# Kernel tuning notes

Measured on AMD Instinct MI355X. Metric: run time of the kernel, lower is better.

## Reference

```python
import jax, jax.numpy as jnp
import numpy as np

N_EMBD = 1024
HEAD_SIZE = 64

def setup_inputs() -> dict:
    key = jax.random.key(0)
    k1, k2, k3, k4 = jax.random.split(key, 4)
    x = jax.random.normal(k1, (8, 2048, N_EMBD), dtype=jnp.float32)
    s = 1.0 / np.sqrt(N_EMBD)
    Wk = jax.random.normal(k2, (HEAD_SIZE, N_EMBD), dtype=jnp.float32) * s
    Wq = jax.random.normal(k3, (HEAD_SIZE, N_EMBD), dtype=jnp.float32) * s
    Wv = jax.random.normal(k4, (HEAD_SIZE, N_EMBD), dtype=jnp.float32) * s
    return {"x": x, "Wk": Wk, "Wq": Wq, "Wv": Wv}

def reference(x, Wk, Wq, Wv):
    B, T, C = x.shape
    k = jnp.einsum('btc,hc->bth', x, Wk)  # [B,T,Hd]
    q = jnp.einsum('btc,hc->bth', x, Wq)
    v = jnp.einsum('btc,hc->bth', x, Wv)
    # NOTE: original scales by C**-0.5 where C = n_embd (not head_size)
    wei = jnp.einsum('bqh,bkh->bqk', q, k) * (C ** -0.5)  # [B,T,T]
    causal = jnp.tril(jnp.ones((T, T), dtype=bool))
    wei = jnp.where(causal, wei, -jnp.inf)
    wei = jax.nn.softmax(wei, axis=-1)
    out = jnp.einsum('bqk,bkh->bqh', wei, v)  # [B,T,Hd]
    return out
```

## Files before the change

kernel.cpp:

```cpp
#include <hip/hip_runtime.h>


typedef __attribute__((ext_vector_type(4))) short sv4;
typedef __attribute__((ext_vector_type(8))) short sv8;
typedef __attribute__((ext_vector_type(4))) float f32x4;

#define NB   8
#define TSEQ 2048
#define CDIM 1024
#define HD   64
#define MROWS (NB * TSEQ)

__device__ __forceinline__ short f2s(float f) {
  union { float f; unsigned u; } v; v.f = f;
  unsigned u = v.u;
  u += 0x7fffu + ((u >> 16) & 1u);
  return (short)(u >> 16);
}
__device__ __forceinline__ unsigned pk2(float lo, float hi) {
  return (unsigned)(unsigned short)f2s(lo) | ((unsigned)(unsigned short)f2s(hi) << 16);
}
__device__ __forceinline__ void glds16(const short* g, short* l) {
  __builtin_amdgcn_global_load_lds(
      (const __attribute__((address_space(1))) unsigned int*)g,
      (__attribute__((address_space(3))) unsigned int*)l, 16, 0, 0);
}

__global__ __launch_bounds__(256) void wcvt(
    const float* __restrict__ Wq, const float* __restrict__ Wk,
    const float* __restrict__ Wv, short* __restrict__ wb)
{
  int i = blockIdx.x * 256 + threadIdx.x;
  int t = i / 3072;
  int rem = i - t * 3072;
  int r = rem >> 4, s = rem & 15;
  int j = r >> 6, wrow = r & 63;
  const float* W = (j == 0) ? Wq : (j == 1) ? Wk : Wv;
  const float* src = W + (size_t)wrow * CDIM + t * 128 + ((s ^ (wrow & 7)) << 3);
  float4 a = *(const float4*)src;
  float4 b = *(const float4*)(src + 4);
  sv8 v = {f2s(a.x), f2s(a.y), f2s(a.z), f2s(a.w),
           f2s(b.x), f2s(b.y), f2s(b.z), f2s(b.w)};
  *(sv8*)(wb + (size_t)i * 8) = v;
}

__global__ __launch_bounds__(1024) void qkv_proj(
    const float* __restrict__ x,
    const short* __restrict__ wb,
    short* __restrict__ qw,
    short* __restrict__ kw,
    short* __restrict__ vtw)
{
  __shared__ short wlds[2][24576];
  __shared__ short xlds[2][8192];
  const int tid  = threadIdx.x;
  const int wid  = tid >> 6;
  const int lane = tid & 63;
  const int g    = lane >> 4;
  const int c16  = lane & 15;
  const int rowg = wid >> 2;
  const int ph   = wid & 3;
  const int row0 = blockIdx.x * 64;

  const int xr = tid >> 4, xs = tid & 15;
  const float* xsrc = x + (size_t)(row0 + xr) * CDIM + xs * 8;
  const int xwo = xr * 128 + ((xs ^ (xr & 7)) << 3);

  const int arow = rowg * 16 + c16;
  const int x7   = arow & 7;
  int rWo[3], rW7[3];
  #pragma unroll
  for (int p6 = 0; p6 < 3; ++p6) {
    int p = ph * 3 + p6;
    int r = (p >> 2) * 64 + (p & 3) * 16 + c16;
    rWo[p6] = r * 128;
    rW7[p6] = r & 7;
  }

  f32x4 acc[3];
  #pragma unroll
  for (int p6 = 0; p6 < 3; ++p6) acc[p6] = (f32x4){0.f, 0.f, 0.f, 0.f};

  float4 px[2][2];

  #pragma unroll
  for (int k2 = 0; k2 < 3; ++k2)
    glds16(wb + (size_t)(tid + k2 * 1024) * 8, &wlds[0][(tid + k2 * 1024) * 8]);
  px[0][0] = *(const float4*)(xsrc);
  px[0][1] = *(const float4*)(xsrc + 4);
  px[1][0] = *(const float4*)(xsrc + 128);
  px[1][1] = *(const float4*)(xsrc + 132);
  asm volatile("s_waitcnt vmcnt(2)" ::: "memory");
  {
    float4 A = px[0][0], B = px[0][1];
    sv8 v = {f2s(A.x), f2s(A.y), f2s(A.z), f2s(A.w),
             f2s(B.x), f2s(B.y), f2s(B.z), f2s(B.w)};
    *(sv8*)&xlds[0][xwo] = v;
  }
  asm volatile("s_waitcnt lgkmcnt(0)" ::: "memory");
  __builtin_amdgcn_sched_barrier(0);
  __builtin_amdgcn_s_barrier();

  #pragma unroll
  for (int t = 0; t < 8; ++t) {
    const int buf = t & 1;
    if (t < 7) {
      #pragma unroll
      for (int k2 = 0; k2 < 3; ++k2)
        glds16(wb + (size_t)((t + 1) * 3072 + tid + k2 * 1024) * 8,
               &wlds[buf ^ 1][(tid + k2 * 1024) * 8]);
    }
    if (t < 6) {
      px[t & 1][0] = *(const float4*)(xsrc + (t + 2) * 128);
      px[t & 1][1] = *(const float4*)(xsrc + (t + 2) * 128 + 4);
    }
    if (t < 7) {
      float4 A = px[(t + 1) & 1][0], B = px[(t + 1) & 1][1];
      sv8 v = {f2s(A.x), f2s(A.y), f2s(A.z), f2s(A.w),
               f2s(B.x), f2s(B.y), f2s(B.z), f2s(B.w)};
      *(sv8*)&xlds[buf ^ 1][xwo] = v;
    }
    #pragma unroll
    for (int kk = 0; kk < 4; ++kk) {
      int kslot = kk * 4 + g;
      sv8 a = *(const sv8*)&xlds[buf][arow * 128 + ((kslot ^ x7) << 3)];
      #pragma unroll
      for (int p6 = 0; p6 < 3; ++p6) {
        sv8 bfr = *(const sv8*)&wlds[buf][rWo[p6] + ((kslot ^ rW7[p6]) << 3)];
        acc[p6] = __builtin_amdgcn_mfma_f32_16x16x32_bf16(a, bfr, acc[p6], 0, 0, 0);
      }
    }
    if (t < 7) {
      if (t < 6) asm volatile("s_waitcnt vmcnt(2) lgkmcnt(0)" ::: "memory");
      else       asm volatile("s_waitcnt vmcnt(0) lgkmcnt(0)" ::: "memory");
      __builtin_amdgcn_sched_barrier(0);
      __builtin_amdgcn_s_barrier();
    }
  }

  #pragma unroll
  for (int p6 = 0; p6 < 3; ++p6) {
    int p = ph * 3 + p6, j = p >> 2, n = p & 3;
    int cc  = (n << 4) + c16;
    int rr0 = row0 + rowg * 16 + (g << 2);
    if (j == 2) {
      int b = rr0 >> 11, ti = rr0 & (TSEQ - 1);
      int kt = ti >> 6, key = ti & 63;
      sv4 v = {f2s(acc[p6][0]), f2s(acc[p6][1]), f2s(acc[p6][2]), f2s(acc[p6][3])};
      *(sv4*)&vtw[(((size_t)b * 32 + kt) * 64 + cc) * 64 +
                  ((((key >> 3) ^ (cc & 7)) << 3) | (key & 7))] = v;
    } else {
      #pragma unroll
      for (int r = 0; r < 4; ++r) {
        int rr = rr0 + r;
        if (j == 0) {
          qw[(size_t)rr * HD + cc] = f2s(acc[p6][r] * 0.03125f);
        } else {
          kw[(size_t)rr * HD + ((((cc >> 3) ^ (rr & 7)) << 3) | (cc & 7))] =
              f2s(acc[p6][r]);
        }
      }
    }
  }
}

__global__ __launch_bounds__(512, 4) void attn(
    const short* __restrict__ qw,
    const short* __restrict__ kw,
    const short* __restrict__ vtw,
    float* __restrict__ Opart,
    float* __restrict__ mlws)
{
  __shared__ short kbuf[2][8192];
  __shared__ short vbuf[2][8192];
  __shared__ short bridge[8][1024];

  const int tid  = threadIdx.x;
  const int wid  = tid >> 6;
  const int lane = tid & 63;
  const int g    = lane >> 4;
  const int c16  = lane & 15;

  const int bid   = blockIdx.x;
  const int batch = bid & 7;
  const int jb    = (bid >> 3) & 15;
  const int qt    = bid >> 7;
  const int q0    = jb << 7;
  const size_t base = (size_t)batch * TSEQ * HD;

  const int ntot = jb + 1;
  const int t0   = (ntot * qt) >> 2;
  const int t1   = (ntot * (qt + 1)) >> 2;

  const int qrow = q0 + (wid << 4) + c16;
  sv8 qa0 = *(const sv8*)(qw + base + (size_t)qrow * HD + (g << 3));
  sv8 qa1 = *(const sv8*)(qw + base + (size_t)qrow * HD + 32 + (g << 3));

  float m = -1e30f, l = 0.f;
  f32x4 o[4];
  #pragma unroll
  for (int n = 0; n < 4; ++n) o[n] = (f32x4){0.f, 0.f, 0.f, 0.f};

  short* br = &bridge[wid][0];
  const int sx7 = c16 & 7;

  #define STAGE(tt, bb)                                                      \
    {                                                                        \
      const short* ksrc = kw + base + (size_t)(tt) * 8192;                   \
      const short* vsrc = vtw + ((size_t)batch * 32 + (tt) * 2) * 4096;      \
      glds16(ksrc + tid * 8,         &kbuf[bb][tid * 8]);                    \
      glds16(ksrc + (512 + tid) * 8, &kbuf[bb][(512 + tid) * 8]);            \
      glds16(vsrc + tid * 8,         &vbuf[bb][tid * 8]);                    \
      glds16(vsrc + (512 + tid) * 8, &vbuf[bb][(512 + tid) * 8]);            \
    }

  if (t0 < t1) {
    STAGE(t0, 0);
    asm volatile("s_waitcnt vmcnt(0)" ::: "memory");
    __builtin_amdgcn_s_barrier();

    for (int t = t0; t < t1; ++t) {
      const int buf = (t - t0) & 1;
      if (t + 1 < t1) STAGE(t + 1, buf ^ 1);

      f32x4 s[8];
      #pragma unroll
      for (int n = 0; n < 8; ++n) s[n] = (f32x4){0.f, 0.f, 0.f, 0.f};
      __builtin_amdgcn_s_setprio(1);
      #pragma unroll
      for (int n = 0; n < 8; ++n) {
        int kr = (n << 4) + c16;
        sv8 k0 = *(const sv8*)&kbuf[buf][kr * 64 + ((g ^ (kr & 7)) << 3)];
        s[n] = __builtin_amdgcn_mfma_f32_16x16x32_bf16(k0, qa0, s[n], 0, 0, 0);
        sv8 k1 = *(const sv8*)&kbuf[buf][kr * 64 + (((4 + g) ^ (kr & 7)) << 3)];
        s[n] = __builtin_amdgcn_mfma_f32_16x16x32_bf16(k1, qa1, s[n], 0, 0, 0);
      }
      __builtin_amdgcn_s_setprio(0);

      if (t == jb) {
        #pragma unroll
        for (int n = 0; n < 8; ++n) {
          int key = (t << 7) + (n << 4) + (g << 2);
          #pragma unroll
          for (int r = 0; r < 4; ++r)
            s[n][r] = (key + r <= qrow) ? s[n][r] : -1e30f;
        }
      }

      float mx = -1e30f;
      #pragma unroll
      for (int n = 0; n < 8; ++n)
        mx = fmaxf(mx, fmaxf(fmaxf(s[n][0], s[n][1]), fmaxf(s[n][2], s[n][3])));
      mx = fmaxf(mx, __shfl_xor(mx, 16));
      mx = fmaxf(mx, __shfl_xor(mx, 32));
      float mnew  = fmaxf(m, mx);
      float alpha = __expf(m - mnew);
      m = mnew;

      float sum = 0.f;
      #pragma unroll
      for (int n = 0; n < 8; ++n) {
        float p0 = __expf(s[n][0] - mnew);
        float p1 = __expf(s[n][1] - mnew);
        float p2 = __expf(s[n][2] - mnew);
        float p3 = __expf(s[n][3] - mnew);
        s[n][0] = p0; s[n][1] = p1; s[n][2] = p2; s[n][3] = p3;
        sum += (p0 + p1) + (p2 + p3);
      }
      sum += __shfl_xor(sum, 16);
      sum += __shfl_xor(sum, 32);
      l = l * alpha + sum;

      float af[4];
      #pragma unroll
      for (int r = 0; r < 4; ++r) af[r] = __shfl(alpha, (g << 2) + r);
      #pragma unroll
      for (int n = 0; n < 4; ++n)
        #pragma unroll
        for (int r = 0; r < 4; ++r) o[n][r] *= af[r];

      #pragma unroll
      for (int hv = 0; hv < 2; ++hv) {
        #pragma unroll
        for (int n = 0; n < 4; ++n) {
          int nn = (hv << 2) + n;
          int slot = 2 * n + (g >> 1);
          uint2 w2;
          w2.x = pk2(s[nn][0], s[nn][1]);
          w2.y = pk2(s[nn][2], s[nn][3]);
          *(uint2*)&br[(c16 << 6) + ((slot ^ sx7) << 3) + ((g & 1) << 2)] = w2;
        }
        asm volatile("s_waitcnt lgkmcnt(0)" ::: "memory");
        __builtin_amdgcn_sched_barrier(0);
        __builtin_amdgcn_s_setprio(1);
        #pragma unroll
        for (int kk = 0; kk < 2; ++kk) {
          int kg    = (hv << 1) + kk;
          int kslot = (kg << 2) + g;
          sv8 pa = *(const sv8*)&br[(c16 << 6) + ((((kk << 2) + g) ^ sx7) << 3)];
          #pragma unroll
          for (int n = 0; n < 4; ++n) {
            int vr = (n << 4) + c16;
            sv8 vf = *(const sv8*)&vbuf[buf][(kslot >> 3) * 4096 + vr * 64 +
                                             (((kslot & 7) ^ (vr & 7)) << 3)];
            o[n] = __builtin_amdgcn_mfma_f32_16x16x32_bf16(pa, vf, o[n], 0, 0, 0);
          }
        }
        __builtin_amdgcn_s_setprio(0);
      }

      if (t + 1 < t1) {
        asm volatile("s_waitcnt vmcnt(0)" ::: "memory");
        __builtin_amdgcn_sched_barrier(0);
        __builtin_amdgcn_s_barrier();
      }
    }
  }

  #pragma unroll
  for (int n = 0; n < 4; ++n) {
    #pragma unroll
    for (int r = 0; r < 4; ++r) {
      int row = (wid << 4) + (g << 2) + r;
      Opart[(size_t)bid * 8192 + row * 64 + (n << 4) + c16] = o[n][r];
    }
  }
  if (lane < 16) {
    int row = (wid << 4) + lane;
    mlws[((size_t)bid * 128 + row) * 2]     = m;
    mlws[((size_t)bid * 128 + row) * 2 + 1] = l;
  }
  #undef STAGE
}

__global__ __launch_bounds__(256) void combine(
    const float* __restrict__ Opart,
    const float* __restrict__ mlws,
    float* __restrict__ out)
{
  const int bid   = blockIdx.x;
  const int batch = bid & 7;
  const int jb    = (bid >> 3) & 15;
  const int half  = bid >> 7;
  const int tid   = threadIdx.x;
  const int row   = (half << 6) + (tid >> 2);
  const int cs    = (tid & 3) << 4;
  const int pb0   = (jb << 3) + batch;

  float mq[4], lq[4];
  #pragma unroll
  for (int q = 0; q < 4; ++q) {
    int pb = (q << 7) + pb0;
    mq[q] = mlws[((size_t)pb * 128 + row) * 2];
    lq[q] = mlws[((size_t)pb * 128 + row) * 2 + 1];
  }
  float M = fmaxf(fmaxf(mq[0], mq[1]), fmaxf(mq[2], mq[3]));
  float w[4], L = 0.f;
  #pragma unroll
  for (int q = 0; q < 4; ++q) { w[q] = __expf(mq[q] - M); L += w[q] * lq[q]; }
  float invL = 1.f / L;

  float* op = out + ((size_t)batch * TSEQ + (jb << 7) + row) * HD + cs;
  #pragma unroll
  for (int e = 0; e < 4; ++e) {
    float4 acc = {0.f, 0.f, 0.f, 0.f};
    #pragma unroll
    for (int q = 0; q < 4; ++q) {
      int pb = (q << 7) + pb0;
      float4 v = *(const float4*)(Opart + (size_t)pb * 8192 + row * 64 + cs + e * 4);
      acc.x += v.x * w[q]; acc.y += v.y * w[q];
      acc.z += v.z * w[q]; acc.w += v.w * w[q];
    }
    acc.x *= invL; acc.y *= invL; acc.z *= invL; acc.w *= invL;
    *(float4*)(op + e * 4) = acc;
  }
}

extern "C" void kernel_launch(void* const* d_in, const int* in_sizes, int n_in,
                              void* d_out, int out_size, void* d_ws, size_t ws_size,
                              hipStream_t stream) {
  const float* x  = (const float*)d_in[0];
  const float* Wk = (const float*)d_in[1];
  const float* Wq = (const float*)d_in[2];
  const float* Wv = (const float*)d_in[3];
  float* out = (float*)d_out;

  short* qw  = (short*)d_ws;
  short* kw  = qw + (size_t)MROWS * HD;
  short* vtw = kw + (size_t)MROWS * HD;
  short* wb  = vtw + (size_t)NB * HD * TSEQ;
  float* Opart = (float*)(wb + 24576 * 8);
  float* mlws  = Opart + (size_t)512 * 8192;

  wcvt<<<dim3(96), dim3(256), 0, stream>>>(Wq, Wk, Wv, wb);
  qkv_proj<<<dim3(MROWS / 64), dim3(1024), 0, stream>>>(x, wb, qw, kw, vtw);
  attn<<<dim3(512), dim3(512), 0, stream>>>(qw, kw, vtw, Opart, mlws);
  combine<<<dim3(256), dim3(256), 0, stream>>>(Opart, mlws, out);
}
```

Before: 52.29 us.

## Give each attention wave two 16-row query tiles, halving block size

The attention block shrinks from 8 waves to 4. Each wave now owns 32 query rows as two 16-row tiles, so every K and V fragment loaded from LDS feeds two MFMAs instead of one. Each thread issues four async K/V copies instead of two, and the P bridge buffer is reorganised per wave. The aim is to cut LDS read traffic per MFMA and raise instruction-level parallelism. The cost is roughly double the accumulator registers per wave and fewer waves to hide latency, which may reduce occupancy.

```diff
diff --git a/kernel.cpp b/kernel.cpp
--- a/kernel.cpp
+++ b/kernel.cpp
@@ -164,7 +164,7 @@
   }
 }
 
-__global__ __launch_bounds__(512, 4) void attn(
+__global__ __launch_bounds__(256) void attn(
     const short* __restrict__ qw,
     const short* __restrict__ kw,
     const short* __restrict__ vtw,
@@ -173,7 +173,7 @@
 {
   __shared__ short kbuf[2][8192];
   __shared__ short vbuf[2][8192];
-  __shared__ short bridge[8][1024];
+  __shared__ short bridge[4][2048];
 
   const int tid  = threadIdx.x;
   const int wid  = tid >> 6;
@@ -192,14 +192,20 @@
   const int t0   = (ntot * qt) >> 2;
   const int t1   = (ntot * (qt + 1)) >> 2;
 
-  const int qrow = q0 + (wid << 4) + c16;
-  sv8 qa0 = *(const sv8*)(qw + base + (size_t)qrow * HD + (g << 3));
-  sv8 qa1 = *(const sv8*)(qw + base + (size_t)qrow * HD + 32 + (g << 3));
-
-  float m = -1e30f, l = 0.f;
-  f32x4 o[4];
-  #pragma unroll
-  for (int n = 0; n < 4; ++n) o[n] = (f32x4){0.f, 0.f, 0.f, 0.f};
+  const int qrA = q0 + (wid << 5) + c16;
+  const int qrB = qrA + 16;
+  sv8 qa0A = *(const sv8*)(qw + base + (size_t)qrA * HD + (g << 3));
+  sv8 qa1A = *(const sv8*)(qw + base + (size_t)qrA * HD + 32 + (g << 3));
+  sv8 qa0B = *(const sv8*)(qw + base + (size_t)qrB * HD + (g << 3));
+  sv8 qa1B = *(const sv8*)(qw + base + (size_t)qrB * HD + 32 + (g << 3));
+
+  float mA = -1e30f, lA = 0.f, mB = -1e30f, lB = 0.f;
+  f32x4 oA[4], oB[4];
+  #pragma unroll
+  for (int n = 0; n < 4; ++n) {
+    oA[n] = (f32x4){0.f, 0.f, 0.f, 0.f};
+    oB[n] = (f32x4){0.f, 0.f, 0.f, 0.f};
+  }
 
   short* br = &bridge[wid][0];
   const int sx7 = c16 & 7;
@@ -208,10 +214,12 @@
     {                                                                        \
       const short* ksrc = kw + base + (size_t)(tt) * 8192;                   \
       const short* vsrc = vtw + ((size_t)batch * 32 + (tt) * 2) * 4096;      \
-      glds16(ksrc + tid * 8,         &kbuf[bb][tid * 8]);                    \
-      glds16(ksrc + (512 + tid) * 8, &kbuf[bb][(512 + tid) * 8]);            \
-      glds16(vsrc + tid * 8,         &vbuf[bb][tid * 8]);                    \
-      glds16(vsrc + (512 + tid) * 8, &vbuf[bb][(512 + tid) * 8]);            \
+      _Pragma("unroll")                                                      \
+      for (int q = 0; q < 4; ++q)                                            \
+        glds16(ksrc + (tid + q * 256) * 8, &kbuf[bb][(tid + q * 256) * 8]);  \
+      _Pragma("unroll")                                                      \
+      for (int q = 0; q < 4; ++q)                                            \
+        glds16(vsrc + (tid + q * 256) * 8, &vbuf[bb][(tid + q * 256) * 8]);  \
     }
 
   if (t0 < t1) {
@@ -223,17 +231,22 @@
       const int buf = (t - t0) & 1;
       if (t + 1 < t1) STAGE(t + 1, buf ^ 1);
 
-      f32x4 s[8];
-      #pragma unroll
-      for (int n = 0; n < 8; ++n) s[n] = (f32x4){0.f, 0.f, 0.f, 0.f};
+      f32x4 sA[8], sB[8];
+      #pragma unroll
+      for (int n = 0; n < 8; ++n) {
+        sA[n] = (f32x4){0.f, 0.f, 0.f, 0.f};
+        sB[n] = (f32x4){0.f, 0.f, 0.f, 0.f};
+      }
       __builtin_amdgcn_s_setprio(1);
       #pragma unroll
       for (int n = 0; n < 8; ++n) {
         int kr = (n << 4) + c16;
         sv8 k0 = *(const sv8*)&kbuf[buf][kr * 64 + ((g ^ (kr & 7)) << 3)];
-        s[n] = __builtin_amdgcn_mfma_f32_16x16x32_bf16(k0, qa0, s[n], 0, 0, 0);
         sv8 k1 = *(const sv8*)&kbuf[buf][kr * 64 + (((4 + g) ^ (kr & 7)) << 3)];
-        s[n] = __builtin_amdgcn_mfma_f32_16x16x32_bf16(k1, qa1, s[n], 0, 0, 0);
+        sA[n] = __builtin_amdgcn_mfma_f32_16x16x32_bf16(k0, qa0A, sA[n], 0, 0, 0);
+        sA[n] = __builtin_amdgcn_mfma_f32_16x16x32_bf16(k1, qa1A, sA[n], 0, 0, 0);
+        sB[n] = __builtin_amdgcn_mfma_f32_16x16x32_bf16(k0, qa0B, sB[n], 0, 0, 0);
+        sB[n] = __builtin_amdgcn_mfma_f32_16x16x32_bf16(k1, qa1B, sB[n], 0, 0, 0);
       }
       __builtin_amdgcn_s_setprio(0);
 
@@ -242,42 +255,58 @@
         for (int n = 0; n < 8; ++n) {
           int key = (t << 7) + (n << 4) + (g << 2);
           #pragma unroll
-          for (int r = 0; r < 4; ++r)
-            s[n][r] = (key + r <= qrow) ? s[n][r] : -1e30f;
-        }
-      }
-
-      float mx = -1e30f;
-      #pragma unroll
-      for (int n = 0; n < 8; ++n)
-        mx = fmaxf(mx, fmaxf(fmaxf(s[n][0], s[n][1]), fmaxf(s[n][2], s[n][3])));
-      mx = fmaxf(mx, __shfl_xor(mx, 16));
-      mx = fmaxf(mx, __shfl_xor(mx, 32));
-      float mnew  = fmaxf(m, mx);
-      float alpha = __expf(m - mnew);
-      m = mnew;
-
-      float sum = 0.f;
+          for (int r = 0; r < 4; ++r) {
+            sA[n][r] = (key + r <= qrA) ? sA[n][r] : -1e30f;
+            sB[n][r] = (key + r <= qrB) ? sB[n][r] : -1e30f;
+          }
+        }
+      }
+
+      float mxA = -1e30f, mxB = -1e30f;
       #pragma unroll
       for (int n = 0; n < 8; ++n) {
-        float p0 = __expf(s[n][0] - mnew);
-        float p1 = __expf(s[n][1] - mnew);
-        float p2 = __expf(s[n][2] - mnew);
-        float p3 = __expf(s[n][3] - mnew);
-        s[n][0] = p0; s[n][1] = p1; s[n][2] = p2; s[n][3] = p3;
-        sum += (p0 + p1) + (p2 + p3);
-      }
-      sum += __shfl_xor(sum, 16);
-      sum += __shfl_xor(sum, 32);
-      l = l * alpha + sum;
-
-      float af[4];
-      #pragma unroll
-      for (int r = 0; r < 4; ++r) af[r] = __shfl(alpha, (g << 2) + r);
+        mxA = fmaxf(mxA, fmaxf(fmaxf(sA[n][0], sA[n][1]), fmaxf(sA[n][2], sA[n][3])));
+        mxB = fmaxf(mxB, fmaxf(fmaxf(sB[n][0], sB[n][1]), fmaxf(sB[n][2], sB[n][3])));
+      }
+      mxA = fmaxf(mxA, __shfl_xor(mxA, 16));
+      mxA = fmaxf(mxA, __shfl_xor(mxA, 32));
+      mxB = fmaxf(mxB, __shfl_xor(mxB, 16));
+      mxB = fmaxf(mxB, __shfl_xor(mxB, 32));
+      float mnA = fmaxf(mA, mxA), mnB = fmaxf(mB, mxB);
+      float alA = __expf(mA - mnA), alB = __expf(mB - mnB);
+      mA = mnA; mB = mnB;
+
+      float sumA = 0.f, sumB = 0.f;
+      #pragma unroll
+      for (int n = 0; n < 8; ++n) {
+        #pragma unroll
+        for (int r = 0; r < 4; ++r) {
+          float pa = __expf(sA[n][r] - mnA);
+          float pb = __expf(sB[n][r] - mnB);
+          sA[n][r] = pa; sB[n][r] = pb;
+          sumA += pa; sumB += pb;
+        }
+      }
+      sumA += __shfl_xor(sumA, 16);
+      sumA += __shfl_xor(sumA, 32);
+      sumB += __shfl_xor(sumB, 16);
+      sumB += __shfl_xor(sumB, 32);
+      lA = lA * alA + sumA;
+      lB = lB * alB + sumB;
+
+      float afA[4], afB[4];
+      #pragma unroll
+      for (int r = 0; r < 4; ++r) {
+        afA[r] = __shfl(alA, (g << 2) + r);
+        afB[r] = __shfl(alB, (g << 2) + r);
+      }
       #pragma unroll
       for (int n = 0; n < 4; ++n)
         #pragma unroll
-        for (int r = 0; r < 4; ++r) o[n][r] *= af[r];
+        for (int r = 0; r < 4; ++r) {
+          oA[n][r] *= afA[r];
+          oB[n][r] *= afB[r];
+        }
 
       #pragma unroll
       for (int hv = 0; hv < 2; ++hv) {
@@ -285,25 +314,29 @@
         for (int n = 0; n < 4; ++n) {
           int nn = (hv << 2) + n;
           int slot = 2 * n + (g >> 1);
-          uint2 w2;
-          w2.x = pk2(s[nn][0], s[nn][1]);
-          w2.y = pk2(s[nn][2], s[nn][3]);
-          *(uint2*)&br[(c16 << 6) + ((slot ^ sx7) << 3) + ((g & 1) << 2)] = w2;
+          int off = (c16 << 6) + ((slot ^ sx7) << 3) + ((g & 1) << 2);
+          uint2 wA, wB;
+          wA.x = pk2(sA[nn][0], sA[nn][1]); wA.y = pk2(sA[nn][2], sA[nn][3]);
+          wB.x = pk2(sB[nn][0], sB[nn][1]); wB.y = pk2(sB[nn][2], sB[nn][3]);
+          *(uint2*)&br[off] = wA;
+          *(uint2*)&br[1024 + off] = wB;
         }
         asm volatile("s_waitcnt lgkmcnt(0)" ::: "memory");
         __builtin_amdgcn_sched_barrier(0);
         __builtin_amdgcn_s_setprio(1);
         #pragma unroll
         for (int kk = 0; kk < 2; ++kk) {
-          int kg    = (hv << 1) + kk;
-          int kslot = (kg << 2) + g;
-          sv8 pa = *(const sv8*)&br[(c16 << 6) + ((((kk << 2) + g) ^ sx7) << 3)];
+          int kslot = (((hv << 1) + kk) << 2) + g;
+          int poff  = (c16 << 6) + ((((kk << 2) + g) ^ sx7) << 3);
+          sv8 paA = *(const sv8*)&br[poff];
+          sv8 paB = *(const sv8*)&br[1024 + poff];
           #pragma unroll
           for (int n = 0; n < 4; ++n) {
             int vr = (n << 4) + c16;
             sv8 vf = *(const sv8*)&vbuf[buf][(kslot >> 3) * 4096 + vr * 64 +
                                              (((kslot & 7) ^ (vr & 7)) << 3)];
-            o[n] = __builtin_amdgcn_mfma_f32_16x16x32_bf16(pa, vf, o[n], 0, 0, 0);
+            oA[n] = __builtin_amdgcn_mfma_f32_16x16x32_bf16(paA, vf, oA[n], 0, 0, 0);
+            oB[n] = __builtin_amdgcn_mfma_f32_16x16x32_bf16(paB, vf, oB[n], 0, 0, 0);
           }
         }
         __builtin_amdgcn_s_setprio(0);
@@ -321,14 +354,17 @@
   for (int n = 0; n < 4; ++n) {
     #pragma unroll
     for (int r = 0; r < 4; ++r) {
-      int row = (wid << 4) + (g << 2) + r;
-      Opart[(size_t)bid * 8192 + row * 64 + (n << 4) + c16] = o[n][r];
+      int rowA = (wid << 5) + (g << 2) + r;
+      Opart[(size_t)bid * 8192 + rowA * 64 + (n << 4) + c16] = oA[n][r];
+      Opart[(size_t)bid * 8192 + (rowA + 16) * 64 + (n << 4) + c16] = oB[n][r];
     }
   }
   if (lane < 16) {
-    int row = (wid << 4) + lane;
-    mlws[((size_t)bid * 128 + row) * 2]     = m;
-    mlws[((size_t)bid * 128 + row) * 2 + 1] = l;
+    int rowA = (wid << 5) + lane;
+    mlws[((size_t)bid * 128 + rowA) * 2]      = mA;
+    mlws[((size_t)bid * 128 + rowA) * 2 + 1]  = lA;
+    mlws[((size_t)bid * 128 + rowA + 16) * 2]     = mB;
+    mlws[((size_t)bid * 128 + rowA + 16) * 2 + 1] = lB;
   }
   #undef STAGE
 }
@@ -394,6 +430,6 @@
 
   wcvt<<<dim3(96), dim3(256), 0, stream>>>(Wq, Wk, Wv, wb);
   qkv_proj<<<dim3(MROWS / 64), dim3(1024), 0, stream>>>(x, wb, qw, kw, vtw);
-  attn<<<dim3(512), dim3(512), 0, stream>>>(qw, kw, vtw, Opart, mlws);
+  attn<<<dim3(512), dim3(256), 0, stream>>>(qw, kw, vtw, Opart, mlws);
   combine<<<dim3(256), dim3(256), 0, stream>>>(Opart, mlws, out);
 }
```

New measurement: 55.40 us. 1.06x slower.
